# Performance work log

Measured on AMD Instinct MI355X. Metric: run time of the kernel, lower is better.

Reference implementation:

```python
import jax, jax.numpy as jnp
import numpy as np

B, S, H = 8, 1024, 768
NUM_HEADS, DH = 12, 64
A, T = 12, 64

def setup_inputs() -> dict:
    key = jax.random.key(0)
    ks = jax.random.split(key, 12)
    all_tokens = jax.random.normal(ks[0], (B, S, H), dtype=jnp.float32)
    aspect_tokens = jax.random.normal(ks[1], (B, A, H), dtype=jnp.float32)
    # ragged target slices: start in [0, S-17), length in [1, 16]
    starts = jax.random.randint(ks[2], (T,), 0, S - 17)
    lens = jax.random.randint(ks[3], (T,), 1, 17)
    target_pos_info = jnp.stack([starts, starts + lens], axis=-1).astype(jnp.int32)  # (T,2)
    target_batch_info = jnp.sort(jax.random.randint(ks[4], (T,), 0, B)).astype(jnp.int32)
    attention_mask = jnp.ones((B, S), dtype=jnp.int32)
    s = 0.02
    W1 = jax.random.normal(ks[5], (H, H), dtype=jnp.float32) * s
    b1 = jnp.zeros((H,), dtype=jnp.float32)
    Wq = jax.random.normal(ks[6], (H, NUM_HEADS, DH), dtype=jnp.float32) * s
    bq = jnp.zeros((NUM_HEADS, DH), dtype=jnp.float32)
    Wk = jax.random.normal(ks[7], (H, NUM_HEADS, DH), dtype=jnp.float32) * s
    bk = jnp.zeros((NUM_HEADS, DH), dtype=jnp.float32)
    Wc = jax.random.normal(ks[8], (2 * H, 1), dtype=jnp.float32) * s
    bc = jnp.zeros((1,), dtype=jnp.float32)
    return {"all_tokens": all_tokens, "aspect_tokens": aspect_tokens,
            "target_pos_info": target_pos_info, "target_batch_info": target_batch_info,
            "attention_mask": attention_mask,
            "W1": W1, "b1": b1, "Wq": Wq, "bq": bq, "Wk": Wk, "bk": bk,
            "Wc": Wc, "bc": bc}


def reference(all_tokens, aspect_tokens, target_pos_info, target_batch_info,
              attention_mask, W1, b1, Wq, bq, Wk, bk, Wc, bc):
    # linear_transform (shared for tokens and aspects), dropout = identity at eval
    h = jax.nn.relu(jnp.einsum('bsh,hg->bsg', all_tokens, W1) + b1)     # (B,S,H)
    # SelfAttention: q/k EinsumDense projections; value = raw key_states reshaped
    q = jnp.einsum('bsh,hkd->bskd', h, Wq) + bq                          # (B,S,K,D)
    k = jnp.einsum('bsh,hkd->bskd', h, Wk) + bk
    v = h.reshape(k.shape)                                               # faithful: reshape, no proj
    q = q * jax.lax.rsqrt(jnp.asarray(DH, q.dtype))
    scores = jnp.einsum('bskd,bqkd->bkqs', k, q)                         # (B,K,Q,S)
    mask_val = attention_mask[:, 0].astype(scores.dtype)                 # original uses mask[:, 0:1]
    scores = scores + ((1.0 - mask_val) * -10000.0)[:, None, None, None]
    probs = jax.nn.softmax(scores, axis=-1)
    out = jnp.einsum('bkqs,bskd->bqkd', probs, v).reshape(h.shape)       # (B,S,H)
    # ragged per-target slice mean: masked mean over positions [s0, s1)
    pos = jnp.arange(S)
    s0, s1 = target_pos_info[:, 0], target_pos_info[:, 1]
    span = ((pos[None, :] >= s0[:, None]) & (pos[None, :] < s1[:, None])).astype(out.dtype)  # (T,S)
    gathered = out[target_batch_info]                                    # (T,S,H)
    counts = jnp.maximum(span.sum(-1, keepdims=True), 1.0)
    rep = jnp.einsum('ts,tsh->th', span, gathered) / counts              # (T,H)
    # aspect hidden states and target-aspect pairing (batch-ordered concat)
    h_a = jax.nn.relu(jnp.einsum('bah,hg->bag', aspect_tokens, W1) + b1)  # (B,A,H)
    pair = jnp.concatenate([jnp.broadcast_to(rep[:, None, :], (rep.shape[0], A, H)),
                            h_a[target_batch_info]], axis=-1)             # (T,A,2H)
    t_a_logit = jnp.einsum('tac,co->tao', pair, Wc) + bc                  # (T,A,1)
    return t_a_logit
```

## Files before the change

kernel.cpp:

```cpp
#include <hip/hip_runtime.h>


typedef __attribute__((ext_vector_type(8))) short s8v;
typedef __attribute__((ext_vector_type(4))) short s4v;
typedef __attribute__((ext_vector_type(4))) float f4v;

#define AS1 __attribute__((address_space(1)))
#define AS3 __attribute__((address_space(3)))

__device__ __forceinline__ unsigned short f2bf(float f) {
  union { float f; unsigned u; } v; v.f = f;
  unsigned r = v.u + 0x7FFFu + ((v.u >> 16) & 1u);
  return (unsigned short)(r >> 16);
}

__device__ __forceinline__ float bf2f(unsigned short u) {
  union { unsigned u; float f; } v; v.u = ((unsigned)u) << 16;
  return v.f;
}

__device__ __forceinline__ void gl2lds16(const void* g, void* l) {
  __builtin_amdgcn_global_load_lds((const AS1 void*)g, (AS3 void*)l, 16, 0, 0);
}

__global__ __launch_bounds__(256) void k_prep(const float* __restrict__ X,
                                              const float* __restrict__ asp,
                                              const float* __restrict__ W1,
                                              const float* __restrict__ Wq,
                                              const float* __restrict__ Wk,
                                              unsigned short* __restrict__ Xbf,
                                              unsigned short* __restrict__ Abf,
                                              unsigned short* __restrict__ W1t,
                                              unsigned short* __restrict__ Wqt,
                                              unsigned short* __restrict__ Wkt) {
  __shared__ float T[64][68];
  int bid = blockIdx.x;
  int tid = threadIdx.x;
  if (bid < 1024) {
    int i = bid * 256 + tid;
    for (; i < 786432; i += 262144) {
      const float4* src = (const float4*)(X + (size_t)i * 8);
      float4 a = src[0], b = src[1];
      s8v o;
      o[0] = (short)f2bf(a.x); o[1] = (short)f2bf(a.y);
      o[2] = (short)f2bf(a.z); o[3] = (short)f2bf(a.w);
      o[4] = (short)f2bf(b.x); o[5] = (short)f2bf(b.y);
      o[6] = (short)f2bf(b.z); o[7] = (short)f2bf(b.w);
      *(s8v*)(Xbf + (size_t)i * 8) = o;
    }
  } else if (bid < 1060) {
    int i = (bid - 1024) * 256 + tid;
    const float4* src = (const float4*)(asp + (size_t)i * 8);
    float4 a = src[0], b = src[1];
    s8v o;
    o[0] = (short)f2bf(a.x); o[1] = (short)f2bf(a.y);
    o[2] = (short)f2bf(a.z); o[3] = (short)f2bf(a.w);
    o[4] = (short)f2bf(b.x); o[5] = (short)f2bf(b.y);
    o[6] = (short)f2bf(b.z); o[7] = (short)f2bf(b.w);
    *(s8v*)(Abf + (size_t)i * 8) = o;
  } else {
    int wb = bid - 1060;
    const float* W = (wb < 144) ? W1 : (wb < 288) ? Wq : Wk;
    unsigned short* Wt = (wb < 144) ? W1t : (wb < 288) ? Wqt : Wkt;
    int tile = wb % 144;
    int tr = (tile / 12) * 64;
    int tc = (tile % 12) * 64;
#pragma unroll
    for (int p = 0; p < 4; ++p) {
      int r = p * 16 + (tid >> 4);
      int c = (tid & 15) * 4;
      float4 v = *(const float4*)(W + (size_t)(tr + r) * 768 + tc + c);
      T[r][c] = v.x; T[r][c + 1] = v.y; T[r][c + 2] = v.z; T[r][c + 3] = v.w;
    }
    __syncthreads();
#pragma unroll
    for (int p = 0; p < 2; ++p) {
      int n = p * 32 + (tid >> 3);
      int k8 = (tid & 7) * 8;
      s8v o;
#pragma unroll
      for (int j = 0; j < 8; ++j) o[j] = (short)f2bf(T[k8 + j][n]);
      *(s8v*)(Wt + (size_t)(tc + n) * 768 + tr + k8) = o;
    }
  }
}

template <int MODE>
__device__ __forceinline__ void gemm_tile(int m0, int n0,
    const unsigned short* __restrict__ A, const unsigned short* __restrict__ Bt,
    const float* __restrict__ bias, unsigned short* __restrict__ C,
    unsigned short* __restrict__ C2, const int* __restrict__ pos,
    const int* __restrict__ tbi, unsigned short* As, unsigned short* Bs,
    int* srcRow) {
  const int K = 768;
  int tid = threadIdx.x, lane = tid & 63, w = tid >> 6;

  if (MODE == 2) {
    if (tid < 64) {
      int r = m0 + tid;
      int t = r >> 4, j = r & 15;
      int s0 = pos[2 * t], s1 = pos[2 * t + 1];
      int s = s0 + j; if (s > s1 - 1) s = s1 - 1;
      srcRow[tid] = tbi[t] * 1024 + s;
    }
    __syncthreads();
  }

  int rsub = lane >> 3;
  int cXor = ((lane & 7) ^ rsub) * 8;
  const unsigned short* aSrc[2];
  const unsigned short* bSrc[4];
#pragma unroll
  for (int i = 0; i < 2; ++i) {
    int lr = (w * 2 + i) * 8 + rsub;
    size_t grow;
    if (MODE == 2) grow = (size_t)srcRow[lr];
    else if (MODE == 3) { int rr = m0 + lr; grow = (size_t)(rr < 96 ? rr : 95); }
    else grow = (size_t)(m0 + lr);
    aSrc[i] = A + grow * K + cXor;
  }
#pragma unroll
  for (int i = 0; i < 4; ++i) {
    int lr = (w * 4 + i) * 8 + rsub;
    bSrc[i] = Bt + (size_t)(n0 + lr) * K + cXor;
  }

  f4v acc[2][4];
#pragma unroll
  for (int i = 0; i < 2; ++i)
#pragma unroll
    for (int j = 0; j < 4; ++j) acc[i][j] = (f4v)(0.0f);

  int wm = (w >> 1) * 32, wn = (w & 1) * 64;
  int lc = lane & 15, lg = lane >> 4;
  int aIdx[2][2], bIdx[4][2];
#pragma unroll
  for (int mi = 0; mi < 2; ++mi) {
    int ra = wm + mi * 16 + lc;
#pragma unroll
    for (int kk = 0; kk < 2; ++kk)
      aIdx[mi][kk] = ra * 64 + (((kk * 4 + lg) ^ (ra & 7)) * 8);
  }
#pragma unroll
  for (int ni = 0; ni < 4; ++ni) {
    int rb = wn + ni * 16 + lc;
#pragma unroll
    for (int kk = 0; kk < 2; ++kk)
      bIdx[ni][kk] = rb * 64 + (((kk * 4 + lg) ^ (rb & 7)) * 8);
  }

  for (int k0 = 0; k0 < K; k0 += 64) {
#pragma unroll
    for (int i = 0; i < 2; ++i) gl2lds16(aSrc[i] + k0, As + (w * 2 + i) * 512);
#pragma unroll
    for (int i = 0; i < 4; ++i) gl2lds16(bSrc[i] + k0, Bs + (w * 4 + i) * 512);
    __syncthreads();
#pragma unroll
    for (int kk = 0; kk < 2; ++kk) {
      s8v ar[2], br[4];
#pragma unroll
      for (int mi = 0; mi < 2; ++mi) ar[mi] = *(const s8v*)(As + aIdx[mi][kk]);
#pragma unroll
      for (int ni = 0; ni < 4; ++ni) br[ni] = *(const s8v*)(Bs + bIdx[ni][kk]);
#pragma unroll
      for (int mi = 0; mi < 2; ++mi)
#pragma unroll
        for (int ni = 0; ni < 4; ++ni)
          acc[mi][ni] = __builtin_amdgcn_mfma_f32_16x16x32_bf16(ar[mi], br[ni], acc[mi][ni], 0, 0, 0);
    }
    __syncthreads();
  }

#pragma unroll
  for (int mi = 0; mi < 2; ++mi) {
#pragma unroll
    for (int ni = 0; ni < 4; ++ni) {
      int col = n0 + wn + ni * 16 + lc;
      float bv = bias[col];
      int row0 = m0 + wm + mi * 16 + lg * 4;
      if (MODE == 0) {
        s4v pk;
#pragma unroll
        for (int r = 0; r < 4; ++r) {
          float x = acc[mi][ni][r] + bv;
          x = x > 0.f ? x : 0.f;
          unsigned short h = f2bf(x);
          pk[r] = (short)h;
          C[(size_t)(row0 + r) * 768 + col] = h;
        }
        int b = row0 >> 10, s = row0 & 1023;
        int kh = col >> 6, d = col & 63;
        *(s4v*)(C2 + ((size_t)((b * 12 + kh) * 64 + d)) * 1024 + s) = pk;
      } else if (MODE == 1) {
#pragma unroll
        for (int r = 0; r < 4; ++r) {
          int row = row0 + r;
          float x = acc[mi][ni][r] + bv;
          int b = row >> 10, s = row & 1023;
          int kh = col >> 6, d = col & 63;
          C[(size_t)((b * 12 + kh) * 1024 + s) * 64 + d] = f2bf(x);
        }
      } else if (MODE == 2) {
#pragma unroll
        for (int r = 0; r < 4; ++r) {
          int row = row0 + r;
          float x = (acc[mi][ni][r] + bv) * 0.125f;
          int t = row >> 4, j = row & 15;
          int kh = col >> 6, d = col & 63;
          C[(size_t)((t * 12 + kh) * 16 + j) * 64 + d] = f2bf(x);
        }
      } else {
#pragma unroll
        for (int r = 0; r < 4; ++r) {
          int row = row0 + r;
          float x = acc[mi][ni][r] + bv;
          x = x > 0.f ? x : 0.f;
          if (row < 96) C[(size_t)row * 768 + col] = f2bf(x);
        }
      }
    }
  }
}

__global__ __launch_bounds__(256) void k_gemmA(const unsigned short* __restrict__ Xbf,
                                               const unsigned short* __restrict__ Abf,
                                               const unsigned short* __restrict__ W1t,
                                               const float* __restrict__ b1,
                                               unsigned short* __restrict__ Hbf,
                                               unsigned short* __restrict__ Vt,
                                               unsigned short* __restrict__ Ha) {
  __shared__ unsigned short As[64 * 64];
  __shared__ unsigned short Bs[128 * 64];
  __shared__ int srcRow[64];
  int bid = blockIdx.x;
  if (bid < 768) {
    bid = (bid & 7) * 96 + (bid >> 3);
    gemm_tile<0>((bid / 6) * 64, (bid % 6) * 128, Xbf, W1t, b1, Hbf, Vt,
                 (const int*)nullptr, (const int*)nullptr, As, Bs, srcRow);
  } else {
    int b2 = bid - 768;
    gemm_tile<3>((b2 / 6) * 64, (b2 % 6) * 128, Abf, W1t, b1, Ha,
                 (unsigned short*)nullptr, (const int*)nullptr, (const int*)nullptr,
                 As, Bs, srcRow);
  }
}

__global__ __launch_bounds__(256) void k_gemmB(const unsigned short* __restrict__ Hbf,
                                               const unsigned short* __restrict__ Wkt,
                                               const float* __restrict__ bk,
                                               unsigned short* __restrict__ Khm,
                                               const unsigned short* __restrict__ Wqt,
                                               const float* __restrict__ bq,
                                               unsigned short* __restrict__ Qhm,
                                               const int* __restrict__ pos,
                                               const int* __restrict__ tbi) {
  __shared__ unsigned short As[64 * 64];
  __shared__ unsigned short Bs[128 * 64];
  __shared__ int srcRow[64];
  int bid = blockIdx.x;
  bid = (bid & 7) * 108 + (bid >> 3);
  if (bid < 768) {
    gemm_tile<1>((bid / 6) * 64, (bid % 6) * 128, Hbf, Wkt, bk, Khm,
                 (unsigned short*)nullptr, (const int*)nullptr, (const int*)nullptr,
                 As, Bs, srcRow);
  } else {
    int b2 = bid - 768;
    gemm_tile<2>((b2 / 6) * 64, (b2 % 6) * 128, Hbf, Wqt, bq, Qhm,
                 (unsigned short*)nullptr, pos, tbi, As, Bs, srcRow);
  }
}

__global__ __launch_bounds__(256) void k_attn(const unsigned short* __restrict__ q_hm,
                                              const unsigned short* __restrict__ k_hm,
                                              const unsigned short* __restrict__ vt,
                                              const int* __restrict__ pos,
                                              const int* __restrict__ tbi,
                                              float* __restrict__ rep) {
  __shared__ unsigned short P[16 * 1032];
  __shared__ float O[4][16][64];
  __shared__ float rsbuf[4][16];
  __shared__ float inv_rs[16];

  int bid = blockIdx.x;
  int t = bid / 12, kh = bid % 12;
  int b = tbi[t];
  int s0 = pos[2 * t], s1 = pos[2 * t + 1];
  int len = s1 - s0;
  int tid = threadIdx.x, lane = tid & 63, w = tid >> 6;
  int lg = lane >> 4, lc = lane & 15;

  const unsigned short* qb = q_hm + (size_t)((t * 12 + kh) * 16) * 64;
  s8v a0 = *(const s8v*)(qb + (size_t)lc * 64 + lg * 8);
  s8v a1 = *(const s8v*)(qb + (size_t)lc * 64 + 32 + lg * 8);

  const unsigned short* kb = k_hm + (size_t)((b * 12 + kh) * 1024) * 64;
  float rs[4] = {0.f, 0.f, 0.f, 0.f};
  for (int it = 0; it < 16; ++it) {
    int sb = it * 64 + w * 16;
    s8v b0 = *(const s8v*)(kb + (size_t)(sb + lc) * 64 + lg * 8);
    s8v b1 = *(const s8v*)(kb + (size_t)(sb + lc) * 64 + 32 + lg * 8);
    f4v c = (f4v)(0.0f);
    c = __builtin_amdgcn_mfma_f32_16x16x32_bf16(a0, b0, c, 0, 0, 0);
    c = __builtin_amdgcn_mfma_f32_16x16x32_bf16(a1, b1, c, 0, 0, 0);
#pragma unroll
    for (int r = 0; r < 4; ++r) {
      float p = __expf(c[r]);
      rs[r] += p;
      P[(lg * 4 + r) * 1032 + sb + lc] = f2bf(p);
    }
  }
#pragma unroll
  for (int m = 1; m < 16; m <<= 1) {
#pragma unroll
    for (int r = 0; r < 4; ++r) rs[r] += __shfl_xor(rs[r], m, 64);
  }
  if (lc == 0) {
#pragma unroll
    for (int r = 0; r < 4; ++r) rsbuf[w][lg * 4 + r] = rs[r];
  }
  __syncthreads();
  if (tid < 16)
    inv_rs[tid] = 1.0f / (rsbuf[0][tid] + rsbuf[1][tid] + rsbuf[2][tid] + rsbuf[3][tid]);

  const unsigned short* vb = vt + (size_t)((b * 12 + kh) * 64) * 1024;
  f4v oc[4];
#pragma unroll
  for (int n = 0; n < 4; ++n) oc[n] = (f4v)(0.0f);
  for (int it = 0; it < 8; ++it) {
    int s32 = it * 128 + w * 32;
    s8v pa = *(const s8v*)(P + lc * 1032 + s32 + lg * 8);
#pragma unroll
    for (int n = 0; n < 4; ++n) {
      s8v vbf = *(const s8v*)(vb + (size_t)(n * 16 + lc) * 1024 + s32 + lg * 8);
      oc[n] = __builtin_amdgcn_mfma_f32_16x16x32_bf16(pa, vbf, oc[n], 0, 0, 0);
    }
  }
#pragma unroll
  for (int n = 0; n < 4; ++n)
#pragma unroll
    for (int r = 0; r < 4; ++r) O[w][lg * 4 + r][n * 16 + lc] = oc[n][r];
  __syncthreads();
  if (tid < 64) {
    float sum = 0.f;
    for (int j = 0; j < len; ++j) {
      float v = O[0][j][tid] + O[1][j][tid] + O[2][j][tid] + O[3][j][tid];
      sum += v * inv_rs[j];
    }
    rep[(size_t)t * 768 + kh * 64 + tid] = sum / (float)len;
  }
}

__global__ __launch_bounds__(256) void k_final(const float* __restrict__ rep,
                                               const unsigned short* __restrict__ ha,
                                               const float* __restrict__ Wc,
                                               const float* __restrict__ bc,
                                               const int* __restrict__ tbi,
                                               float* __restrict__ out) {
  __shared__ float red[4];
  __shared__ float hadot[12];
  int t = blockIdx.x, tid = threadIdx.x;
  int lane = tid & 63, w = tid >> 6;
  int b = tbi[t];
  float part = 0.f;
#pragma unroll
  for (int gi = 0; gi < 3; ++gi) {
    int g = tid + gi * 256;
    part += rep[(size_t)t * 768 + g] * Wc[g];
  }
#pragma unroll
  for (int m = 1; m < 64; m <<= 1) part += __shfl_xor(part, m, 64);
  if (lane == 0) red[w] = part;
#pragma unroll
  for (int j = 0; j < 3; ++j) {
    int a = w * 3 + j;
    const unsigned short* hr = ha + (size_t)(b * 12 + a) * 768;
    float p2 = 0.f;
#pragma unroll
    for (int q = 0; q < 12; ++q) {
      int g = lane + q * 64;
      p2 += bf2f(hr[g]) * Wc[768 + g];
    }
#pragma unroll
    for (int m = 1; m < 64; m <<= 1) p2 += __shfl_xor(p2, m, 64);
    if (lane == 0) hadot[a] = p2;
  }
  __syncthreads();
  float ra = red[0] + red[1] + red[2] + red[3];
  if (tid < 12) out[t * 12 + tid] = ra + hadot[tid] + bc[0];
}

extern "C" void kernel_launch(void* const* d_in, const int* in_sizes, int n_in,
                              void* d_out, int out_size, void* d_ws, size_t ws_size,
                              hipStream_t stream) {
  const float* all_tokens = (const float*)d_in[0];
  const float* aspect     = (const float*)d_in[1];
  const int*   pos        = (const int*)d_in[2];
  const int*   tbi        = (const int*)d_in[3];
  const float* W1 = (const float*)d_in[5];
  const float* b1 = (const float*)d_in[6];
  const float* Wq = (const float*)d_in[7];
  const float* bq = (const float*)d_in[8];
  const float* Wk = (const float*)d_in[9];
  const float* bk = (const float*)d_in[10];
  const float* Wc = (const float*)d_in[11];
  const float* bc = (const float*)d_in[12];
  float* out = (float*)d_out;

  char* ws = (char*)d_ws;
  unsigned short* Xbf = (unsigned short*)(ws);
  unsigned short* W1t = (unsigned short*)(ws + 12582912);
  unsigned short* Wqt = (unsigned short*)(ws + 13762560);
  unsigned short* Wkt = (unsigned short*)(ws + 14942208);
  unsigned short* Hbf = (unsigned short*)(ws + 16121856);
  unsigned short* Khm = (unsigned short*)(ws + 28704768);
  unsigned short* Vt  = (unsigned short*)(ws + 41287680);
  unsigned short* Qhm = (unsigned short*)(ws + 53870592);
  float* Rep = (float*)(ws + 55443456);
  unsigned short* Abf = (unsigned short*)(ws + 55640448);
  unsigned short* Ha  = (unsigned short*)(ws + 55787904);

  hipLaunchKernelGGL(k_prep, dim3(1492), dim3(256), 0, stream,
                     all_tokens, aspect, W1, Wq, Wk, Xbf, Abf, W1t, Wqt, Wkt);
  hipLaunchKernelGGL(k_gemmA, dim3(780), dim3(256), 0, stream,
                     Xbf, Abf, W1t, b1, Hbf, Vt, Ha);
  hipLaunchKernelGGL(k_gemmB, dim3(864), dim3(256), 0, stream,
                     Hbf, Wkt, bk, Khm, Wqt, bq, Qhm, pos, tbi);
  hipLaunchKernelGGL(k_attn, dim3(768), dim3(256), 0, stream, Qhm, Khm, Vt, pos, tbi, Rep);
  hipLaunchKernelGGL(k_final, dim3(64), dim3(256), 0, stream, Rep, Ha, Wc, bc, tbi, out);
}
```

Before: 80.71 us.

## Double-buffer GEMM LDS tiles and prefetch K/V operands in attention

The shared GEMM tile loop now double-buffers its A and B LDS tiles. It issues the direct global-to-LDS loads for the next k-step before computing the current one, and uses explicit vmcnt waits and barriers instead of full __syncthreads around each step. The attention kernel software-pipelines its K and V/P operand loads into registers one iteration ahead, raises wave priority around the MFMA groups, and swizzles block indices across the eight batches. The goal is to hide global memory latency behind matrix-core work. In exchange, LDS per GEMM block doubles to about 48KB, which may reduce occupancy, and the GEMM loop count is now hardcoded to twelve steps (K=768).

```diff
diff --git a/kernel.cpp b/kernel.cpp
--- a/kernel.cpp
+++ b/kernel.cpp
@@ -149,26 +149,45 @@
       bIdx[ni][kk] = rb * 64 + (((kk * 4 + lg) ^ (rb & 7)) * 8);
   }
 
-  for (int k0 = 0; k0 < K; k0 += 64) {
-#pragma unroll
-    for (int i = 0; i < 2; ++i) gl2lds16(aSrc[i] + k0, As + (w * 2 + i) * 512);
-#pragma unroll
-    for (int i = 0; i < 4; ++i) gl2lds16(bSrc[i] + k0, Bs + (w * 4 + i) * 512);
-    __syncthreads();
+#pragma unroll
+  for (int i = 0; i < 2; ++i) gl2lds16(aSrc[i], As + (w * 2 + i) * 512);
+#pragma unroll
+  for (int i = 0; i < 4; ++i) gl2lds16(bSrc[i], Bs + (w * 4 + i) * 512);
+
+  for (int t = 0; t < 12; ++t) {
+    int cur = t & 1;
+    int nxt = 1 - cur;
+    if (t < 11) {
+      int k0 = (t + 1) * 64;
+#pragma unroll
+      for (int i = 0; i < 2; ++i)
+        gl2lds16(aSrc[i] + k0, As + nxt * 4096 + (w * 2 + i) * 512);
+#pragma unroll
+      for (int i = 0; i < 4; ++i)
+        gl2lds16(bSrc[i] + k0, Bs + nxt * 8192 + (w * 4 + i) * 512);
+      asm volatile("s_waitcnt vmcnt(6)" ::: "memory");
+    } else {
+      asm volatile("s_waitcnt vmcnt(0)" ::: "memory");
+    }
+    __builtin_amdgcn_s_barrier();
+    __builtin_amdgcn_sched_barrier(0);
 #pragma unroll
     for (int kk = 0; kk < 2; ++kk) {
       s8v ar[2], br[4];
 #pragma unroll
-      for (int mi = 0; mi < 2; ++mi) ar[mi] = *(const s8v*)(As + aIdx[mi][kk]);
-#pragma unroll
-      for (int ni = 0; ni < 4; ++ni) br[ni] = *(const s8v*)(Bs + bIdx[ni][kk]);
+      for (int mi = 0; mi < 2; ++mi)
+        ar[mi] = *(const s8v*)(As + cur * 4096 + aIdx[mi][kk]);
+#pragma unroll
+      for (int ni = 0; ni < 4; ++ni)
+        br[ni] = *(const s8v*)(Bs + cur * 8192 + bIdx[ni][kk]);
 #pragma unroll
       for (int mi = 0; mi < 2; ++mi)
 #pragma unroll
         for (int ni = 0; ni < 4; ++ni)
           acc[mi][ni] = __builtin_amdgcn_mfma_f32_16x16x32_bf16(ar[mi], br[ni], acc[mi][ni], 0, 0, 0);
     }
-    __syncthreads();
+    __builtin_amdgcn_sched_barrier(0);
+    __builtin_amdgcn_s_barrier();
   }
 
 #pragma unroll
@@ -229,8 +248,8 @@
                                                unsigned short* __restrict__ Hbf,
                                                unsigned short* __restrict__ Vt,
                                                unsigned short* __restrict__ Ha) {
-  __shared__ unsigned short As[64 * 64];
-  __shared__ unsigned short Bs[128 * 64];
+  __shared__ unsigned short As[2 * 4096];
+  __shared__ unsigned short Bs[2 * 8192];
   __shared__ int srcRow[64];
   int bid = blockIdx.x;
   if (bid < 768) {
@@ -254,8 +273,8 @@
                                                unsigned short* __restrict__ Qhm,
                                                const int* __restrict__ pos,
                                                const int* __restrict__ tbi) {
-  __shared__ unsigned short As[64 * 64];
-  __shared__ unsigned short Bs[128 * 64];
+  __shared__ unsigned short As[2 * 4096];
+  __shared__ unsigned short Bs[2 * 8192];
   __shared__ int srcRow[64];
   int bid = blockIdx.x;
   bid = (bid & 7) * 108 + (bid >> 3);
@@ -282,6 +301,7 @@
   __shared__ float inv_rs[16];
 
   int bid = blockIdx.x;
+  bid = (bid & 7) * 96 + (bid >> 3);
   int t = bid / 12, kh = bid % 12;
   int b = tbi[t];
   int s0 = pos[2 * t], s1 = pos[2 * t + 1];
@@ -295,19 +315,28 @@
 
   const unsigned short* kb = k_hm + (size_t)((b * 12 + kh) * 1024) * 64;
   float rs[4] = {0.f, 0.f, 0.f, 0.f};
+  s8v b0 = *(const s8v*)(kb + (size_t)(w * 16 + lc) * 64 + lg * 8);
+  s8v b1 = *(const s8v*)(kb + (size_t)(w * 16 + lc) * 64 + 32 + lg * 8);
   for (int it = 0; it < 16; ++it) {
+    s8v nb0, nb1;
+    if (it < 15) {
+      int sn = (it + 1) * 64 + w * 16;
+      nb0 = *(const s8v*)(kb + (size_t)(sn + lc) * 64 + lg * 8);
+      nb1 = *(const s8v*)(kb + (size_t)(sn + lc) * 64 + 32 + lg * 8);
+    }
     int sb = it * 64 + w * 16;
-    s8v b0 = *(const s8v*)(kb + (size_t)(sb + lc) * 64 + lg * 8);
-    s8v b1 = *(const s8v*)(kb + (size_t)(sb + lc) * 64 + 32 + lg * 8);
     f4v c = (f4v)(0.0f);
+    __builtin_amdgcn_s_setprio(1);
     c = __builtin_amdgcn_mfma_f32_16x16x32_bf16(a0, b0, c, 0, 0, 0);
     c = __builtin_amdgcn_mfma_f32_16x16x32_bf16(a1, b1, c, 0, 0, 0);
+    __builtin_amdgcn_s_setprio(0);
 #pragma unroll
     for (int r = 0; r < 4; ++r) {
       float p = __expf(c[r]);
       rs[r] += p;
       P[(lg * 4 + r) * 1032 + sb + lc] = f2bf(p);
     }
+    b0 = nb0; b1 = nb1;
   }
 #pragma unroll
   for (int m = 1; m < 16; m <<= 1) {
@@ -326,14 +355,28 @@
   f4v oc[4];
 #pragma unroll
   for (int n = 0; n < 4; ++n) oc[n] = (f4v)(0.0f);
+  s8v pa = *(const s8v*)(P + lc * 1032 + w * 32 + lg * 8);
+  s8v vb0 = *(const s8v*)(vb + (size_t)(0 * 16 + lc) * 1024 + w * 32 + lg * 8);
+  s8v vb1 = *(const s8v*)(vb + (size_t)(1 * 16 + lc) * 1024 + w * 32 + lg * 8);
+  s8v vb2 = *(const s8v*)(vb + (size_t)(2 * 16 + lc) * 1024 + w * 32 + lg * 8);
+  s8v vb3 = *(const s8v*)(vb + (size_t)(3 * 16 + lc) * 1024 + w * 32 + lg * 8);
   for (int it = 0; it < 8; ++it) {
-    int s32 = it * 128 + w * 32;
-    s8v pa = *(const s8v*)(P + lc * 1032 + s32 + lg * 8);
-#pragma unroll
-    for (int n = 0; n < 4; ++n) {
-      s8v vbf = *(const s8v*)(vb + (size_t)(n * 16 + lc) * 1024 + s32 + lg * 8);
-      oc[n] = __builtin_amdgcn_mfma_f32_16x16x32_bf16(pa, vbf, oc[n], 0, 0, 0);
-    }
+    s8v pan, vn0, vn1, vn2, vn3;
+    if (it < 7) {
+      int sn = (it + 1) * 128 + w * 32;
+      pan = *(const s8v*)(P + lc * 1032 + sn + lg * 8);
+      vn0 = *(const s8v*)(vb + (size_t)(0 * 16 + lc) * 1024 + sn + lg * 8);
+      vn1 = *(const s8v*)(vb + (size_t)(1 * 16 + lc) * 1024 + sn + lg * 8);
+      vn2 = *(const s8v*)(vb + (size_t)(2 * 16 + lc) * 1024 + sn + lg * 8);
+      vn3 = *(const s8v*)(vb + (size_t)(3 * 16 + lc) * 1024 + sn + lg * 8);
+    }
+    __builtin_amdgcn_s_setprio(1);
+    oc[0] = __builtin_amdgcn_mfma_f32_16x16x32_bf16(pa, vb0, oc[0], 0, 0, 0);
+    oc[1] = __builtin_amdgcn_mfma_f32_16x16x32_bf16(pa, vb1, oc[1], 0, 0, 0);
+    oc[2] = __builtin_amdgcn_mfma_f32_16x16x32_bf16(pa, vb2, oc[2], 0, 0, 0);
+    oc[3] = __builtin_amdgcn_mfma_f32_16x16x32_bf16(pa, vb3, oc[3], 0, 0, 0);
+    __builtin_amdgcn_s_setprio(0);
+    pa = pan; vb0 = vn0; vb1 = vn1; vb2 = vn2; vb3 = vn3;
   }
 #pragma unroll
   for (int n = 0; n < 4; ++n)
```

Result: slower. 87.70 us (+8.7%).

## Double-buffer LDS tiles in GEMM k-loop and remap attention block order

Applied to the files above, without the earlier changes.

The GEMM tile loop now prefetches the next K-slice into a second LDS buffer via global_load_lds while computing MFMAs on the current one, using one barrier per iteration instead of two. This is meant to hide global load latency behind compute. LDS use doubles to 48KB per block, which may reduce occupancy. The attention kernel also remaps block IDs in an XCD-style swizzle (bid&7)*96+(bid>>3), which assumes 768 blocks.

```diff
diff --git a/kernel.cpp b/kernel.cpp
--- a/kernel.cpp
+++ b/kernel.cpp
@@ -149,26 +149,43 @@
       bIdx[ni][kk] = rb * 64 + (((kk * 4 + lg) ^ (rb & 7)) * 8);
   }
 
-  for (int k0 = 0; k0 < K; k0 += 64) {
-#pragma unroll
-    for (int i = 0; i < 2; ++i) gl2lds16(aSrc[i] + k0, As + (w * 2 + i) * 512);
-#pragma unroll
-    for (int i = 0; i < 4; ++i) gl2lds16(bSrc[i] + k0, Bs + (w * 4 + i) * 512);
-    __syncthreads();
+#pragma unroll
+  for (int i = 0; i < 2; ++i) gl2lds16(aSrc[i], As + (w * 2 + i) * 512);
+#pragma unroll
+  for (int i = 0; i < 4; ++i) gl2lds16(bSrc[i], Bs + (w * 4 + i) * 512);
+  asm volatile("s_waitcnt vmcnt(0)" ::: "memory");
+  __builtin_amdgcn_s_barrier();
+
+  for (int t = 0; t < 12; ++t) {
+    int cur = t & 1, nxt = cur ^ 1;
+    if (t < 11) {
+      int k0 = (t + 1) * 64;
+#pragma unroll
+      for (int i = 0; i < 2; ++i)
+        gl2lds16(aSrc[i] + k0, As + nxt * 4096 + (w * 2 + i) * 512);
+#pragma unroll
+      for (int i = 0; i < 4; ++i)
+        gl2lds16(bSrc[i] + k0, Bs + nxt * 8192 + (w * 4 + i) * 512);
+    }
 #pragma unroll
     for (int kk = 0; kk < 2; ++kk) {
       s8v ar[2], br[4];
 #pragma unroll
-      for (int mi = 0; mi < 2; ++mi) ar[mi] = *(const s8v*)(As + aIdx[mi][kk]);
-#pragma unroll
-      for (int ni = 0; ni < 4; ++ni) br[ni] = *(const s8v*)(Bs + bIdx[ni][kk]);
+      for (int mi = 0; mi < 2; ++mi)
+        ar[mi] = *(const s8v*)(As + cur * 4096 + aIdx[mi][kk]);
+#pragma unroll
+      for (int ni = 0; ni < 4; ++ni)
+        br[ni] = *(const s8v*)(Bs + cur * 8192 + bIdx[ni][kk]);
 #pragma unroll
       for (int mi = 0; mi < 2; ++mi)
 #pragma unroll
         for (int ni = 0; ni < 4; ++ni)
           acc[mi][ni] = __builtin_amdgcn_mfma_f32_16x16x32_bf16(ar[mi], br[ni], acc[mi][ni], 0, 0, 0);
     }
-    __syncthreads();
+    if (t < 11) {
+      asm volatile("s_waitcnt vmcnt(0)" ::: "memory");
+      __builtin_amdgcn_s_barrier();
+    }
   }
 
 #pragma unroll
@@ -229,8 +246,8 @@
                                                unsigned short* __restrict__ Hbf,
                                                unsigned short* __restrict__ Vt,
                                                unsigned short* __restrict__ Ha) {
-  __shared__ unsigned short As[64 * 64];
-  __shared__ unsigned short Bs[128 * 64];
+  __shared__ unsigned short As[2 * 4096];
+  __shared__ unsigned short Bs[2 * 8192];
   __shared__ int srcRow[64];
   int bid = blockIdx.x;
   if (bid < 768) {
@@ -254,8 +271,8 @@
                                                unsigned short* __restrict__ Qhm,
                                                const int* __restrict__ pos,
                                                const int* __restrict__ tbi) {
-  __shared__ unsigned short As[64 * 64];
-  __shared__ unsigned short Bs[128 * 64];
+  __shared__ unsigned short As[2 * 4096];
+  __shared__ unsigned short Bs[2 * 8192];
   __shared__ int srcRow[64];
   int bid = blockIdx.x;
   bid = (bid & 7) * 108 + (bid >> 3);
@@ -282,6 +299,7 @@
   __shared__ float inv_rs[16];
 
   int bid = blockIdx.x;
+  bid = (bid & 7) * 96 + (bid >> 3);
   int t = bid / 12, kh = bid % 12;
   int b = tbi[t];
   int s0 = pos[2 * t], s1 = pos[2 * t + 1];
```

Result: slower. 103.0 us (+27.6%).

## Fuse final classifier into attention kernel via atomics; flatten prep grid

Applied to the files above, without the earlier changes.

The separate k_final kernel is removed. Each attention block now reduces its head's slice of rep against Wc and, for its kh-indexed aspect, the aspect dot product, then atomically adds partial logits into the output, which is zeroed by a memset first. The prep kernel gives one block per conversion chunk instead of a grid-stride loop, and attention blocks are remapped with an XCD-style swizzle. This saves a kernel launch and the rep round trip through memory, at the cost of a memset, float atomics with nondeterministic summation order, and a larger prep grid.

```diff
diff --git a/kernel.cpp b/kernel.cpp
--- a/kernel.cpp
+++ b/kernel.cpp
@@ -36,20 +36,18 @@
   __shared__ float T[64][68];
   int bid = blockIdx.x;
   int tid = threadIdx.x;
-  if (bid < 1024) {
+  if (bid < 3072) {
     int i = bid * 256 + tid;
-    for (; i < 786432; i += 262144) {
-      const float4* src = (const float4*)(X + (size_t)i * 8);
-      float4 a = src[0], b = src[1];
-      s8v o;
-      o[0] = (short)f2bf(a.x); o[1] = (short)f2bf(a.y);
-      o[2] = (short)f2bf(a.z); o[3] = (short)f2bf(a.w);
-      o[4] = (short)f2bf(b.x); o[5] = (short)f2bf(b.y);
-      o[6] = (short)f2bf(b.z); o[7] = (short)f2bf(b.w);
-      *(s8v*)(Xbf + (size_t)i * 8) = o;
-    }
-  } else if (bid < 1060) {
-    int i = (bid - 1024) * 256 + tid;
+    const float4* src = (const float4*)(X + (size_t)i * 8);
+    float4 a = src[0], b = src[1];
+    s8v o;
+    o[0] = (short)f2bf(a.x); o[1] = (short)f2bf(a.y);
+    o[2] = (short)f2bf(a.z); o[3] = (short)f2bf(a.w);
+    o[4] = (short)f2bf(b.x); o[5] = (short)f2bf(b.y);
+    o[6] = (short)f2bf(b.z); o[7] = (short)f2bf(b.w);
+    *(s8v*)(Xbf + (size_t)i * 8) = o;
+  } else if (bid < 3108) {
+    int i = (bid - 3072) * 256 + tid;
     const float4* src = (const float4*)(asp + (size_t)i * 8);
     float4 a = src[0], b = src[1];
     s8v o;
@@ -59,7 +57,7 @@
     o[6] = (short)f2bf(b.z); o[7] = (short)f2bf(b.w);
     *(s8v*)(Abf + (size_t)i * 8) = o;
   } else {
-    int wb = bid - 1060;
+    int wb = bid - 3108;
     const float* W = (wb < 144) ? W1 : (wb < 288) ? Wq : Wk;
     unsigned short* Wt = (wb < 144) ? W1t : (wb < 288) ? Wqt : Wkt;
     int tile = wb % 144;
@@ -273,15 +271,21 @@
 __global__ __launch_bounds__(256) void k_attn(const unsigned short* __restrict__ q_hm,
                                               const unsigned short* __restrict__ k_hm,
                                               const unsigned short* __restrict__ vt,
+                                              const unsigned short* __restrict__ ha,
                                               const int* __restrict__ pos,
                                               const int* __restrict__ tbi,
-                                              float* __restrict__ rep) {
+                                              const float* __restrict__ Wc,
+                                              const float* __restrict__ bc,
+                                              float* __restrict__ outp) {
   __shared__ unsigned short P[16 * 1032];
   __shared__ float O[4][16][64];
   __shared__ float rsbuf[4][16];
   __shared__ float inv_rs[16];
+  __shared__ float hpart[4];
+  __shared__ float rabuf;
 
   int bid = blockIdx.x;
+  bid = (bid & 7) * 96 + (bid >> 3);
   int t = bid / 12, kh = bid % 12;
   int b = tbi[t];
   int s0 = pos[2 * t], s1 = pos[2 * t + 1];
@@ -340,53 +344,36 @@
 #pragma unroll
     for (int r = 0; r < 4; ++r) O[w][lg * 4 + r][n * 16 + lc] = oc[n][r];
   __syncthreads();
-  if (tid < 64) {
+  if (w == 0) {
     float sum = 0.f;
     for (int j = 0; j < len; ++j) {
-      float v = O[0][j][tid] + O[1][j][tid] + O[2][j][tid] + O[3][j][tid];
+      float v = O[0][j][lane] + O[1][j][lane] + O[2][j][lane] + O[3][j][lane];
       sum += v * inv_rs[j];
     }
-    rep[(size_t)t * 768 + kh * 64 + tid] = sum / (float)len;
-  }
-}
-
-__global__ __launch_bounds__(256) void k_final(const float* __restrict__ rep,
-                                               const unsigned short* __restrict__ ha,
-                                               const float* __restrict__ Wc,
-                                               const float* __restrict__ bc,
-                                               const int* __restrict__ tbi,
-                                               float* __restrict__ out) {
-  __shared__ float red[4];
-  __shared__ float hadot[12];
-  int t = blockIdx.x, tid = threadIdx.x;
-  int lane = tid & 63, w = tid >> 6;
-  int b = tbi[t];
-  float part = 0.f;
-#pragma unroll
-  for (int gi = 0; gi < 3; ++gi) {
-    int g = tid + gi * 256;
-    part += rep[(size_t)t * 768 + g] * Wc[g];
-  }
-#pragma unroll
-  for (int m = 1; m < 64; m <<= 1) part += __shfl_xor(part, m, 64);
-  if (lane == 0) red[w] = part;
-#pragma unroll
-  for (int j = 0; j < 3; ++j) {
-    int a = w * 3 + j;
-    const unsigned short* hr = ha + (size_t)(b * 12 + a) * 768;
+    float repd = sum / (float)len;
+    float pr = repd * Wc[kh * 64 + lane];
+#pragma unroll
+    for (int m = 1; m < 64; m <<= 1) pr += __shfl_xor(pr, m, 64);
+    if (lane == 0) rabuf = pr;
+  } else {
+    const unsigned short* hr = ha + (size_t)(b * 12 + kh) * 768;
     float p2 = 0.f;
 #pragma unroll
-    for (int q = 0; q < 12; ++q) {
-      int g = lane + q * 64;
+    for (int q = 0; q < 4; ++q) {
+      int g = (tid - 64) + q * 192;
       p2 += bf2f(hr[g]) * Wc[768 + g];
     }
 #pragma unroll
     for (int m = 1; m < 64; m <<= 1) p2 += __shfl_xor(p2, m, 64);
-    if (lane == 0) hadot[a] = p2;
+    if (lane == 0) hpart[w] = p2;
   }
   __syncthreads();
-  float ra = red[0] + red[1] + red[2] + red[3];
-  if (tid < 12) out[t * 12 + tid] = ra + hadot[tid] + bc[0];
+  if (tid < 12) {
+    float ra = rabuf;
+    float had = hpart[1] + hpart[2] + hpart[3];
+    float v = ra + ((tid == kh) ? (had + bc[0]) : 0.f);
+    atomicAdd(&outp[t * 12 + tid], v);
+  }
 }
 
 extern "C" void kernel_launch(void* const* d_in, const int* in_sizes, int n_in,
@@ -415,16 +402,16 @@
   unsigned short* Khm = (unsigned short*)(ws + 28704768);
   unsigned short* Vt  = (unsigned short*)(ws + 41287680);
   unsigned short* Qhm = (unsigned short*)(ws + 53870592);
-  float* Rep = (float*)(ws + 55443456);
   unsigned short* Abf = (unsigned short*)(ws + 55640448);
   unsigned short* Ha  = (unsigned short*)(ws + 55787904);
 
-  hipLaunchKernelGGL(k_prep, dim3(1492), dim3(256), 0, stream,
+  hipMemsetAsync(out, 0, (size_t)out_size * sizeof(float), stream);
+  hipLaunchKernelGGL(k_prep, dim3(3540), dim3(256), 0, stream,
                      all_tokens, aspect, W1, Wq, Wk, Xbf, Abf, W1t, Wqt, Wkt);
   hipLaunchKernelGGL(k_gemmA, dim3(780), dim3(256), 0, stream,
                      Xbf, Abf, W1t, b1, Hbf, Vt, Ha);
   hipLaunchKernelGGL(k_gemmB, dim3(864), dim3(256), 0, stream,
                      Hbf, Wkt, bk, Khm, Wqt, bq, Qhm, pos, tbi);
-  hipLaunchKernelGGL(k_attn, dim3(768), dim3(256), 0, stream, Qhm, Khm, Vt, pos, tbi, Rep);
-  hipLaunchKernelGGL(k_final, dim3(64), dim3(256), 0, stream, Rep, Ha, Wc, bc, tbi, out);
-}
+  hipLaunchKernelGGL(k_attn, dim3(768), dim3(256), 0, stream,
+                     Qhm, Khm, Vt, Ha, pos, tbi, Wc, bc, out);
+}
```

New measurement: 84.77 us. 5.0% more time.
